# Kernel optimization log

Hardware: AMD Instinct MI355X
Metric: run time of the kernel (lower is better)

The kernel has to match this reference:

```python
import jax, jax.numpy as jnp
import numpy as np

# FP4 E2M1 magnitude lookup table (3-bit magnitude index)
FP4_LUT = jnp.array([0.0, 0.5, 1.0, 1.5, 2.0, 3.0, 4.0, 6.0], dtype=jnp.float32)
E8M0_BIAS = 127


def setup_inputs() -> dict:
    key = jax.random.key(0)
    k_in, k_pw, k_sc, k_b = jax.random.split(key, 4)
    B, S, I, O, BS = 4, 2048, 4096, 11008, 32
    inp = jax.random.normal(k_in, (B, S, I), dtype=jnp.float32)
    # packed MXFP4 codes: two 4-bit codes per byte
    packed_weight = jax.random.randint(k_pw, (O, I // 2), 0, 256, dtype=jnp.int32)
    # E8M0 exponents near the bias so dequantized magnitudes are O(1)
    weight_scales = jax.random.randint(k_sc, (O, I // BS), 118, 132, dtype=jnp.int32)
    bias = jax.random.normal(k_b, (O,), dtype=jnp.float32) * 0.02
    return {"input": inp, "bias": bias, "packed_weight": packed_weight,
            "weight_scales": weight_scales}


def _dequantize_mxfp4(packed_weight, weight_scales):
    O, P = packed_weight.shape
    I = P * 2
    bs = I // weight_scales.shape[1]
    lo = packed_weight & 0xF          # first element of each pair: low nibble
    hi = (packed_weight >> 4) & 0xF   # second element: high nibble
    codes = jnp.stack([lo, hi], axis=-1).reshape(O, I)  # [O, I]
    mag = FP4_LUT[codes & 0x7]
    sign = jnp.where((codes & 0x8) > 0, -1.0, 1.0)
    vals = sign * mag                                   # [O, I] fp4 values
    scale = jnp.exp2((weight_scales - E8M0_BIAS).astype(jnp.float32))  # [O, I/bs]
    w = (vals.reshape(O, I // bs, bs) * scale[:, :, None]).reshape(O, I)
    return w


def reference(input, bias, packed_weight, weight_scales):
    # quantized-inference path: on-the-fly block dequant + F.linear
    w = _dequantize_mxfp4(packed_weight, weight_scales)  # [O, I]
    out = jnp.einsum('bsi,oi->bso', input, w) + bias     # [B, S, O]
    return out
```

## Files before the change

### kernel.cpp

```cpp
#include <hip/hip_runtime.h>
#include <stdint.h>

typedef __attribute__((ext_vector_type(8))) short bf16x8;
typedef __attribute__((ext_vector_type(8))) unsigned short u16x8;
typedef __attribute__((ext_vector_type(16))) float f32x16;
typedef __attribute__((ext_vector_type(4))) int i32x4;

static constexpr int MDIM = 8192;
static constexpr int KDIM = 4096;
static constexpr int NDIM = 11008;
static constexpr int BM = 256, BN = 256, BK = 32;
static constexpr int NBX = NDIM / BN;
static constexpr int NBY = MDIM / BM;


static __device__ __forceinline__ unsigned short f2bf(float f) {
  unsigned int u = __builtin_bit_cast(unsigned int, f);
  return (unsigned short)((u + 0x7FFFu + ((u >> 16) & 1u)) >> 16);
}

static __device__ __forceinline__ float fp4_val(unsigned int c) {
  unsigned int m = c & 1u, e = (c >> 1) & 3u, s = (c >> 3) & 1u;
  unsigned int bits = e ? (((126u + e) << 23) | (m << 22)) : (m ? 0x3F000000u : 0u);
  bits |= s << 31;
  return __builtin_bit_cast(float, bits);
}

static constexpr int CONV_BLOCKS = (MDIM * KDIM / 8) / 256;
static constexpr int DEQ_BLOCKS  = (NDIM * (KDIM / 32)) / 256;

__global__ __launch_bounds__(256) void prep_kernel(
    const float4* __restrict__ in, u16x8* __restrict__ aout,
    const int* __restrict__ pw, const int* __restrict__ sc,
    unsigned short* __restrict__ wout) {
  if (blockIdx.x < CONV_BLOCKS) {
    int i = blockIdx.x * 256 + threadIdx.x;
    float4 v0 = in[2 * (size_t)i];
    float4 v1 = in[2 * (size_t)i + 1];
    u16x8 r;
    r[0] = f2bf(v0.x); r[1] = f2bf(v0.y); r[2] = f2bf(v0.z); r[3] = f2bf(v0.w);
    r[4] = f2bf(v1.x); r[5] = f2bf(v1.y); r[6] = f2bf(v1.z); r[7] = f2bf(v1.w);
    aout[i] = r;
  } else {
    int tid = (blockIdx.x - CONV_BLOCKS) * 256 + threadIdx.x;
    int o = tid >> 7;
    int b = tid & 127;
    const i32x4* src = (const i32x4*)(pw + (size_t)o * (KDIM / 2) + b * 16);
    unsigned int e = (unsigned int)sc[(size_t)o * (KDIM / 32) + b];
    float scale = __builtin_bit_cast(float, e << 23);
    unsigned short* dst = wout + (size_t)o * KDIM + b * 32;
#pragma unroll
    for (int v = 0; v < 4; ++v) {
      i32x4 w4 = src[v];
      u16x8 r;
#pragma unroll
      for (int j = 0; j < 4; ++j) {
        unsigned int w = (unsigned int)w4[j];
        r[2 * j]     = f2bf(fp4_val(w & 0xFu) * scale);
        r[2 * j + 1] = f2bf(fp4_val((w >> 4) & 0xFu) * scale);
      }
      *(u16x8*)(dst + 8 * v) = r;
    }
  }
}


#define GLDS16(gp, lp)                                                                  \
  __builtin_amdgcn_global_load_lds((const __attribute__((address_space(1))) void*)(gp), \
                                   (__attribute__((address_space(3))) void*)(lp), 16, 0, 0)

#define BAR() asm volatile("s_barrier" ::: "memory")

template <int SLOT, bool STAGE, int VN>
__device__ __forceinline__ void ktile(
    unsigned char* lds, const unsigned short*& gA, const unsigned short*& gB,
    int stq, int aBase, int bBase, int kof0, int kof1, f32x16 (&acc)[4][2]) {
  if constexpr (VN == 8)      asm volatile("s_waitcnt vmcnt(8)" ::: "memory");
  else if constexpr (VN == 4) asm volatile("s_waitcnt vmcnt(4)" ::: "memory");
  else                        asm volatile("s_waitcnt vmcnt(0)" ::: "memory");
  BAR();
  if (STAGE) {
    unsigned char* da = lds + ((SLOT + 3) & 3) * 32768 + stq;
    GLDS16(gA, da);
    GLDS16(gA + (size_t)128 * KDIM, da + 8192);
    GLDS16(gB, da + 16384);
    GLDS16(gB + (size_t)128 * KDIM, da + 24576);
    gA += BK; gB += BK;
  }
  const unsigned char* sa = lds + SLOT * 32768;
  const unsigned char* sb = sa + 16384;
  bf16x8 a[4], b[2];
#pragma unroll
  for (int mf = 0; mf < 4; ++mf) a[mf] = *(const bf16x8*)(sa + aBase + mf * 2048 + kof0);
#pragma unroll
  for (int nf = 0; nf < 2; ++nf) b[nf] = *(const bf16x8*)(sb + bBase + nf * 2048 + kof0);
  __builtin_amdgcn_s_setprio(1);
#pragma unroll
  for (int mf = 0; mf < 4; ++mf)
#pragma unroll
    for (int nf = 0; nf < 2; ++nf)
      acc[mf][nf] = __builtin_amdgcn_mfma_f32_32x32x16_bf16(a[mf], b[nf], acc[mf][nf], 0, 0, 0);
  __builtin_amdgcn_s_setprio(0);
#pragma unroll
  for (int mf = 0; mf < 4; ++mf) a[mf] = *(const bf16x8*)(sa + aBase + mf * 2048 + kof1);
#pragma unroll
  for (int nf = 0; nf < 2; ++nf) b[nf] = *(const bf16x8*)(sb + bBase + nf * 2048 + kof1);
  __builtin_amdgcn_s_setprio(1);
#pragma unroll
  for (int mf = 0; mf < 4; ++mf)
#pragma unroll
    for (int nf = 0; nf < 2; ++nf)
      acc[mf][nf] = __builtin_amdgcn_mfma_f32_32x32x16_bf16(a[mf], b[nf], acc[mf][nf], 0, 0, 0);
  __builtin_amdgcn_s_setprio(0);
}

__global__ __launch_bounds__(512, 2) void gemm_mx_kernel(
    const unsigned short* __restrict__ A,
    const unsigned short* __restrict__ Bw,
    const float* __restrict__ bias,
    float* __restrict__ C) {
  __shared__ __align__(16) unsigned char lds[4 * 32768];

  const int t = threadIdx.x;
  const int lane = t & 63;
  const int wave = t >> 6;
  const int wr = wave >> 2;
  const int wc = wave & 3;

  const int bid = blockIdx.x;
  const int swb = (bid & 7) * ((NBX * NBY) / 8) + (bid >> 3);
  const int by = swb / NBX;
  const int bx = swb - by * NBX;
  const int m0 = by * BM, n0 = bx * BN;

  const int rl = lane & 31;
  const int hi = lane >> 5;
  const int kof0 = ((0 + hi) ^ ((rl >> 1) & 3)) * 16;
  const int kof1 = ((2 + hi) ^ ((rl >> 1) & 3)) * 16;
  const int aBase = (wr * 128 + rl) * 64;
  const int bBase = (wc * 64 + rl) * 64;

  const int stq = t * 16;
  const int srow = t >> 2;
  const int koff = 8 * ((t & 3) ^ ((t >> 3) & 3));
  const unsigned short* gA = A + (size_t)(m0 + srow) * KDIM + koff;
  const unsigned short* gB = Bw + (size_t)(n0 + srow) * KDIM + koff;

  f32x16 acc[4][2] = {};

#pragma unroll
  for (int p = 0; p < 3; ++p) {
    unsigned char* da = lds + p * 32768 + stq;
    GLDS16(gA, da);
    GLDS16(gA + (size_t)128 * KDIM, da + 8192);
    GLDS16(gB, da + 16384);
    GLDS16(gB + (size_t)128 * KDIM, da + 24576);
    gA += BK; gB += BK;
  }

  for (int it = 0; it < 31; ++it) {
    ktile<0, true, 8>(lds, gA, gB, stq, aBase, bBase, kof0, kof1, acc);
    ktile<1, true, 8>(lds, gA, gB, stq, aBase, bBase, kof0, kof1, acc);
    ktile<2, true, 8>(lds, gA, gB, stq, aBase, bBase, kof0, kof1, acc);
    ktile<3, true, 8>(lds, gA, gB, stq, aBase, bBase, kof0, kof1, acc);
  }
  ktile<0, true, 8>(lds, gA, gB, stq, aBase, bBase, kof0, kof1, acc);
  ktile<1, false, 8>(lds, gA, gB, stq, aBase, bBase, kof0, kof1, acc);
  ktile<2, false, 4>(lds, gA, gB, stq, aBase, bBase, kof0, kof1, acc);
  ktile<3, false, 0>(lds, gA, gB, stq, aBase, bBase, kof0, kof1, acc);

#pragma unroll
  for (int nf = 0; nf < 2; ++nf) {
    const int gn = n0 + wc * 64 + nf * 32 + rl;
    const float bv = bias[gn];
#pragma unroll
    for (int mf = 0; mf < 4; ++mf) {
      const int base = m0 + wr * 128 + mf * 32 + 4 * hi;
#pragma unroll
      for (int q = 0; q < 4; ++q) {
        float* cp = C + (size_t)(base + 8 * q) * NDIM + gn;
#pragma unroll
        for (int rr = 0; rr < 4; ++rr)
          cp[(size_t)rr * NDIM] = acc[mf][nf][q * 4 + rr] + bv;
      }
    }
  }
}

extern "C" void kernel_launch(void* const* d_in, const int* in_sizes, int n_in,
                              void* d_out, int out_size, void* d_ws, size_t ws_size,
                              hipStream_t stream) {
  const float* inp  = (const float*)d_in[0];
  const float* bias = (const float*)d_in[1];
  const int* pw     = (const int*)d_in[2];
  const int* sc     = (const int*)d_in[3];
  float* out = (float*)d_out;

  unsigned short* a_bf = (unsigned short*)d_ws;
  unsigned short* w_bf = a_bf + (size_t)MDIM * KDIM;
  size_t need = ((size_t)MDIM * KDIM + (size_t)NDIM * KDIM) * sizeof(unsigned short);
  if (ws_size < need) return;

  prep_kernel<<<dim3(CONV_BLOCKS + DEQ_BLOCKS), dim3(256), 0, stream>>>(
      (const float4*)inp, (u16x8*)a_bf, pw, sc, w_bf);
  gemm_mx_kernel<<<dim3(NBX * NBY), dim3(512), 0, stream>>>(a_bf, w_bf, bias, out);
}
```

Baseline: 859.0 us.

## Switch to 16x16x32 MFMA with register double-buffered LDS fragment prefetch

Replaces the 32x32x16 bf16 MFMA tiling with 16x16x32 MFMAs over an 8x4 fragment grid per wave. LDS fragments for the next K-tile are read into alternating register buffers while the current tile's MFMAs issue, and the wait plus barrier move to the end of each tile. The aim is to hide LDS read latency behind matrix work and cut the stalls between barrier and MFMA issue. The cost is higher register pressure from the two fragment buffers plus the extra A fragments, which could spill or lower occupancy under the 512-thread, 2-blocks bound. The prefetch-then-barrier ordering is also trickier to keep correct.

```diff
diff --git a/kernel.cpp b/kernel.cpp
--- a/kernel.cpp
+++ b/kernel.cpp
@@ -3,7 +3,7 @@
 
 typedef __attribute__((ext_vector_type(8))) short bf16x8;
 typedef __attribute__((ext_vector_type(8))) unsigned short u16x8;
-typedef __attribute__((ext_vector_type(16))) float f32x16;
+typedef __attribute__((ext_vector_type(4))) float f32x4;
 typedef __attribute__((ext_vector_type(4))) int i32x4;
 
 static constexpr int MDIM = 8192;
@@ -71,14 +71,11 @@
 
 #define BAR() asm volatile("s_barrier" ::: "memory")
 
-template <int SLOT, bool STAGE, int VN>
+template <int SLOT, bool STAGE, int VN, bool NEXTREAD>
 __device__ __forceinline__ void ktile(
     unsigned char* lds, const unsigned short*& gA, const unsigned short*& gB,
-    int stq, int aBase, int bBase, int kof0, int kof1, f32x16 (&acc)[4][2]) {
-  if constexpr (VN == 8)      asm volatile("s_waitcnt vmcnt(8)" ::: "memory");
-  else if constexpr (VN == 4) asm volatile("s_waitcnt vmcnt(4)" ::: "memory");
-  else                        asm volatile("s_waitcnt vmcnt(0)" ::: "memory");
-  BAR();
+    int stq, int aBase, int bBase, int kof,
+    bf16x8 (&cur)[8], bf16x8 (&nxt)[8], bf16x8 (&a2)[4], f32x4 (&acc)[8][4]) {
   if (STAGE) {
     unsigned char* da = lds + ((SLOT + 3) & 3) * 32768 + stq;
     GLDS16(gA, da);
@@ -87,31 +84,33 @@
     GLDS16(gB + (size_t)128 * KDIM, da + 24576);
     gA += BK; gB += BK;
   }
-  const unsigned char* sa = lds + SLOT * 32768;
+  const unsigned char* sa = lds + ((SLOT + 1) & 3) * 32768;
   const unsigned char* sb = sa + 16384;
-  bf16x8 a[4], b[2];
-#pragma unroll
-  for (int mf = 0; mf < 4; ++mf) a[mf] = *(const bf16x8*)(sa + aBase + mf * 2048 + kof0);
-#pragma unroll
-  for (int nf = 0; nf < 2; ++nf) b[nf] = *(const bf16x8*)(sb + bBase + nf * 2048 + kof0);
+  if (NEXTREAD) {
+#pragma unroll
+    for (int m = 0; m < 4; ++m) nxt[m] = *(const bf16x8*)(sa + aBase + m * 1024 + kof);
+#pragma unroll
+    for (int n = 0; n < 4; ++n) nxt[4 + n] = *(const bf16x8*)(sb + bBase + n * 1024 + kof);
+  }
   __builtin_amdgcn_s_setprio(1);
 #pragma unroll
-  for (int mf = 0; mf < 4; ++mf)
-#pragma unroll
-    for (int nf = 0; nf < 2; ++nf)
-      acc[mf][nf] = __builtin_amdgcn_mfma_f32_32x32x16_bf16(a[mf], b[nf], acc[mf][nf], 0, 0, 0);
+  for (int m = 0; m < 4; ++m)
+#pragma unroll
+    for (int n = 0; n < 4; ++n)
+      acc[m][n] = __builtin_amdgcn_mfma_f32_16x16x32_bf16(cur[m], cur[4 + n], acc[m][n], 0, 0, 0);
+#pragma unroll
+  for (int m = 0; m < 4; ++m)
+#pragma unroll
+    for (int n = 0; n < 4; ++n)
+      acc[4 + m][n] = __builtin_amdgcn_mfma_f32_16x16x32_bf16(a2[m], cur[4 + n], acc[4 + m][n], 0, 0, 0);
   __builtin_amdgcn_s_setprio(0);
-#pragma unroll
-  for (int mf = 0; mf < 4; ++mf) a[mf] = *(const bf16x8*)(sa + aBase + mf * 2048 + kof1);
-#pragma unroll
-  for (int nf = 0; nf < 2; ++nf) b[nf] = *(const bf16x8*)(sb + bBase + nf * 2048 + kof1);
-  __builtin_amdgcn_s_setprio(1);
-#pragma unroll
-  for (int mf = 0; mf < 4; ++mf)
-#pragma unroll
-    for (int nf = 0; nf < 2; ++nf)
-      acc[mf][nf] = __builtin_amdgcn_mfma_f32_32x32x16_bf16(a[mf], b[nf], acc[mf][nf], 0, 0, 0);
-  __builtin_amdgcn_s_setprio(0);
+  if (NEXTREAD) {
+#pragma unroll
+    for (int m = 0; m < 4; ++m) a2[m] = *(const bf16x8*)(sa + aBase + (4 + m) * 1024 + kof);
+  }
+  if (VN == 4) asm volatile("s_waitcnt vmcnt(4)" ::: "memory");
+  else         asm volatile("s_waitcnt vmcnt(0)" ::: "memory");
+  BAR();
 }
 
 __global__ __launch_bounds__(512, 2) void gemm_mx_kernel(
@@ -133,12 +132,11 @@
   const int bx = swb - by * NBX;
   const int m0 = by * BM, n0 = bx * BN;
 
-  const int rl = lane & 31;
-  const int hi = lane >> 5;
-  const int kof0 = ((0 + hi) ^ ((rl >> 1) & 3)) * 16;
-  const int kof1 = ((2 + hi) ^ ((rl >> 1) & 3)) * 16;
-  const int aBase = (wr * 128 + rl) * 64;
-  const int bBase = (wc * 64 + rl) * 64;
+  const int fl = lane & 15;
+  const int fh = lane >> 4;
+  const int kof = (fh ^ ((fl >> 1) & 3)) * 16;
+  const int aBase = (wr * 128 + fl) * 64;
+  const int bBase = (wc * 64 + fl) * 64;
 
   const int stq = t * 16;
   const int srow = t >> 2;
@@ -146,7 +144,8 @@
   const unsigned short* gA = A + (size_t)(m0 + srow) * KDIM + koff;
   const unsigned short* gB = Bw + (size_t)(n0 + srow) * KDIM + koff;
 
-  f32x16 acc[4][2] = {};
+  f32x4 acc[8][4] = {};
+  bf16x8 r0[8], r1[8], a2[4];
 
 #pragma unroll
   for (int p = 0; p < 3; ++p) {
@@ -157,32 +156,41 @@
     GLDS16(gB + (size_t)128 * KDIM, da + 24576);
     gA += BK; gB += BK;
   }
+  asm volatile("s_waitcnt vmcnt(4)" ::: "memory");
+  BAR();
+  {
+    const unsigned char* sa = lds;
+    const unsigned char* sb = lds + 16384;
+#pragma unroll
+    for (int m = 0; m < 4; ++m) r0[m] = *(const bf16x8*)(sa + aBase + m * 1024 + kof);
+#pragma unroll
+    for (int n = 0; n < 4; ++n) r0[4 + n] = *(const bf16x8*)(sb + bBase + n * 1024 + kof);
+#pragma unroll
+    for (int m = 0; m < 4; ++m) a2[m] = *(const bf16x8*)(sa + aBase + (4 + m) * 1024 + kof);
+  }
 
   for (int it = 0; it < 31; ++it) {
-    ktile<0, true, 8>(lds, gA, gB, stq, aBase, bBase, kof0, kof1, acc);
-    ktile<1, true, 8>(lds, gA, gB, stq, aBase, bBase, kof0, kof1, acc);
-    ktile<2, true, 8>(lds, gA, gB, stq, aBase, bBase, kof0, kof1, acc);
-    ktile<3, true, 8>(lds, gA, gB, stq, aBase, bBase, kof0, kof1, acc);
-  }
-  ktile<0, true, 8>(lds, gA, gB, stq, aBase, bBase, kof0, kof1, acc);
-  ktile<1, false, 8>(lds, gA, gB, stq, aBase, bBase, kof0, kof1, acc);
-  ktile<2, false, 4>(lds, gA, gB, stq, aBase, bBase, kof0, kof1, acc);
-  ktile<3, false, 0>(lds, gA, gB, stq, aBase, bBase, kof0, kof1, acc);
-
-#pragma unroll
-  for (int nf = 0; nf < 2; ++nf) {
-    const int gn = n0 + wc * 64 + nf * 32 + rl;
+    ktile<0, true, 4, true>(lds, gA, gB, stq, aBase, bBase, kof, r0, r1, a2, acc);
+    ktile<1, true, 4, true>(lds, gA, gB, stq, aBase, bBase, kof, r1, r0, a2, acc);
+    ktile<2, true, 4, true>(lds, gA, gB, stq, aBase, bBase, kof, r0, r1, a2, acc);
+    ktile<3, true, 4, true>(lds, gA, gB, stq, aBase, bBase, kof, r1, r0, a2, acc);
+  }
+  ktile<0, true, 4, true>(lds, gA, gB, stq, aBase, bBase, kof, r0, r1, a2, acc);
+  ktile<1, false, 0, true>(lds, gA, gB, stq, aBase, bBase, kof, r1, r0, a2, acc);
+  ktile<2, false, 0, true>(lds, gA, gB, stq, aBase, bBase, kof, r0, r1, a2, acc);
+  ktile<3, false, 0, false>(lds, gA, gB, stq, aBase, bBase, kof, r1, r0, a2, acc);
+
+#pragma unroll
+  for (int n = 0; n < 4; ++n) {
+    const int gn = n0 + wc * 64 + n * 16 + fl;
     const float bv = bias[gn];
 #pragma unroll
-    for (int mf = 0; mf < 4; ++mf) {
-      const int base = m0 + wr * 128 + mf * 32 + 4 * hi;
-#pragma unroll
-      for (int q = 0; q < 4; ++q) {
-        float* cp = C + (size_t)(base + 8 * q) * NDIM + gn;
-#pragma unroll
-        for (int rr = 0; rr < 4; ++rr)
-          cp[(size_t)rr * NDIM] = acc[mf][nf][q * 4 + rr] + bv;
-      }
+    for (int m = 0; m < 8; ++m) {
+      const int gm = m0 + wr * 128 + m * 16 + fh * 4;
+      float* cp = C + (size_t)gm * NDIM + gn;
+#pragma unroll
+      for (int r = 0; r < 4; ++r)
+        cp[(size_t)r * NDIM] = acc[m][n][r] + bv;
     }
   }
 }
```

New measurement: 829.9 us. 3.4% less time.
